# Performance work log

Measured on AMD Instinct MI355X. Metric: run time of the kernel, lower is better.

Reference implementation:

```python
import jax, jax.numpy as jnp
import numpy as np

GROUPS = 64; SIDE = 8; STEPS = 8
TAU = 1.0; FLOOR = 1e-4; EPS = 1e-4
MU = 1.0; DT = 0.1; GAMMA = 0.1
FLOW_W = 1.0; LOCAL_W = 0.5; KEEP_RATIO = 0.5


def _with_floor(m):
    n = m.shape[-1]
    mask = 1.0 - jnp.eye(n, dtype=m.dtype)
    return jnp.maximum(m * mask, FLOOR * mask)


def _norm_scores(s):
    mean = s.mean(axis=1, keepdims=True)
    std = jnp.clip(s.std(axis=1, ddof=1, keepdims=True), 1e-6, None)  # torch unbiased std
    return (s - mean) / std


def _router_core(tokens, cls_token, W, grid_h, grid_w):
    B, P, D = tokens.shape
    # group ids from patch grid position (patch_indices defaults to arange)
    pi = jnp.broadcast_to(jnp.arange(P), (B, P))
    row, col = pi // grid_w, pi % grid_w
    gh = -(-grid_h // SIDE); gw = -(-grid_w // SIDE)  # ceil div
    gid = jnp.minimum(row // gh, SIDE - 1) * SIDE + jnp.minimum(col // gw, SIDE - 1)  # [B,P]
    # mean-pool tokens per group (scatter_add + count)
    seg = jax.vmap(lambda t, g: jax.ops.segment_sum(t, g, num_segments=GROUPS))
    grouped = seg(tokens, gid)                                 # [B,G,D]
    counts = seg(jnp.ones((B, P, 1), tokens.dtype), gid)       # [B,G,1]
    grouped = grouped / jnp.maximum(counts, 1.0)
    nodes = jnp.concatenate([cls_token[:, None, :], grouped], axis=1)  # [B,G+1,D]
    # pairwise conductance: project, l2-normalize, squared cdist, exp kernel
    proj = jnp.einsum('bnd,ed->bne', nodes, W)  # Linear (no bias): x @ W.T
    proj = proj / jnp.maximum(jnp.linalg.norm(proj, axis=-1, keepdims=True), 1e-12)
    sq = jnp.sum(proj * proj, axis=-1)
    d2 = jnp.maximum(sq[:, :, None] + sq[:, None, :]
                     - 2.0 * jnp.einsum('bnd,bmd->bnm', proj, proj), 0.0)
    C = _with_floor(jnp.exp(-d2 / TAU))
    C = 0.5 * (C + jnp.swapaxes(C, -1, -2))  # symmetric
    # source: cls node injects, groups drain
    source = jnp.full((B, GROUPS + 1), -1.0 / GROUPS, C.dtype).at[:, 0].set(1.0)
    N = GROUPS + 1
    I = jnp.eye(N, dtype=C.dtype)
    d_list, q_list = [C], []
    for _ in range(STEPS):
        deg = C.sum(-1)
        system = deg[:, :, None] * I - C + EPS * I            # Laplacian + eps*I
        p = jnp.linalg.solve(system, source[..., None])[..., 0]
        flow = C * (p[:, :, None] - p[:, None, :])
        q_list.append(flow)
        r = jnp.abs(flow) ** MU
        r = r / (1.0 + r)
        C = C + DT * (r - GAMMA * C)
        C = _with_floor(jnp.maximum(C, 0.0))
        C = _with_floor(0.5 * (C + jnp.swapaxes(C, -1, -2)))
        d_list.append(C)
    return C, jnp.stack(d_list, 1), jnp.stack(q_list, 1), gid


def setup_inputs() -> dict:
    key = jax.random.key(0)
    k1, k2, k3, k4 = jax.random.split(key, 4)
    B, P, D = 64, 576, 768
    return {
        'tokens': jax.random.normal(k1, (B, P, D), jnp.float32),
        'cls_token': jax.random.normal(k2, (B, D), jnp.float32),
        'W': jax.random.normal(k3, (D, D), jnp.float32) / np.sqrt(D),
        'local_scores': jax.random.normal(k4, (B, P), jnp.float32),
        'grid_h': 24,
        'grid_w': 24,
    }


def reference(tokens, cls_token, W, local_scores, grid_h, grid_w):
    B, P, _ = tokens.shape
    final_d, d_hist, q_hist, gid = _router_core(tokens, cls_token, W, grid_h, grid_w)
    routing = final_d[:, 1:, 1:]
    routing = routing / jnp.clip(routing.sum(-1, keepdims=True), 1e-6, None)
    group_flow = jnp.abs(q_hist[:, -1, 1:, :]).sum(-1)        # [B,G]
    group_scores = jnp.take_along_axis(_norm_scores(group_flow), gid, axis=1)
    token_scores = FLOW_W * group_scores + LOCAL_W * _norm_scores(local_scores)
    keep_count = max(1, int(round(P * KEEP_RATIO)))
    _, topk = jax.lax.top_k(token_scores, keep_count)
    patch_keep_mask = jnp.zeros((B, P), bool).at[jnp.arange(B)[:, None], topk].set(True)
    keep_mask = jnp.concatenate([jnp.ones((B, 1), bool), patch_keep_mask], axis=1)
    delta = d_hist[:, 1:] - d_hist[:, :-1]
    aux_sparse = final_d[:, 1:, 1:].sum(axis=(-1, -2)).mean()
    aux_stable = jnp.abs(delta).sum(axis=(-1, -2, -3)).mean()
    return (keep_mask, patch_keep_mask, gid, group_scores, d_hist, q_hist,
            routing, aux_sparse, aux_stable)
```

## Files before the change

kernel.cpp:

```cpp
#include <hip/hip_runtime.h>
#include <stdint.h>

#define NB 64
#define NP 576
#define ND 768
#define NG 64
#define NN 65
#define NSTEPS 8
#define FLOORV 1.0e-4f
#define EPSV   1.0e-4f
#define DTV    0.1f
#define GAMMAV 0.1f
#define KEEPC  288
#define PITCH2 68

__global__ __launch_bounds__(256) void k_group_means(const float* __restrict__ tokens,
                                                     const float* __restrict__ cls,
                                                     float* __restrict__ nodes,
                                                     const int* __restrict__ ghp,
                                                     const int* __restrict__ gwp) {
    int bx = blockIdx.x;
    int b = bx / NN, n = bx - b * NN;
    int tid = threadIdx.x;
    float* orow = nodes + (size_t)bx * ND;
    if (n == 0) {
        for (int d = tid; d < ND; d += 256) orow[d] = cls[(size_t)b * ND + d];
        return;
    }
    int grid_h = *ghp, grid_w = *gwp;
    int gh = (grid_h + 7) / 8, gw = (grid_w + 7) / 8;
    int g = n - 1, gr = g >> 3, gc = g & 7;
    int r0 = gr * gh, r1 = (gr == 7) ? grid_h : min((gr + 1) * gh, grid_h);
    int c0 = gc * gw, c1 = (gc == 7) ? grid_w : min((gc + 1) * gw, grid_w);
    int cnt = (r1 > r0 && c1 > c0) ? (r1 - r0) * (c1 - c0) : 0;
    float cf = (float)max(cnt, 1);
    const float* tb = tokens + (size_t)b * NP * ND;
    for (int d = tid; d < ND; d += 256) {
        float acc = 0.f;
        for (int r = r0; r < r1; ++r)
            for (int c = c0; c < c1; ++c)
                acc += tb[(size_t)(r * grid_w + c) * ND + d];
        orow[d] = acc / cf;
    }
}

__global__ __launch_bounds__(256) void k_gemm_nt(const float* __restrict__ A,
                                                 const float* __restrict__ Bm,
                                                 float* __restrict__ Cm) {
    __shared__ float As[32][68];
    __shared__ float Bs[32][68];
    int tid = threadIdx.x;
    int m0 = blockIdx.x * 64, n0 = blockIdx.y * 64;
    int tx = tid & 15, ty = tid >> 4;
    float acc[4][4];
#pragma unroll
    for (int i = 0; i < 4; ++i)
#pragma unroll
        for (int j = 0; j < 4; ++j) acc[i][j] = 0.f;
    int lrow = tid >> 3, lq = tid & 7;
    for (int k0 = 0; k0 < ND; k0 += 32) {
#pragma unroll
        for (int l = 0; l < 2; ++l) {
            int row = lrow + l * 32;
            float4 va = *(const float4*)&A[(size_t)(m0 + row) * ND + k0 + lq * 4];
            As[lq * 4 + 0][row] = va.x; As[lq * 4 + 1][row] = va.y;
            As[lq * 4 + 2][row] = va.z; As[lq * 4 + 3][row] = va.w;
            float4 vb = *(const float4*)&Bm[(size_t)(n0 + row) * ND + k0 + lq * 4];
            Bs[lq * 4 + 0][row] = vb.x; Bs[lq * 4 + 1][row] = vb.y;
            Bs[lq * 4 + 2][row] = vb.z; Bs[lq * 4 + 3][row] = vb.w;
        }
        __syncthreads();
#pragma unroll
        for (int kk = 0; kk < 32; ++kk) {
            float4 a4 = *(const float4*)&As[kk][ty * 4];
            float4 b4 = *(const float4*)&Bs[kk][tx * 4];
            float av[4] = {a4.x, a4.y, a4.z, a4.w};
            float bv[4] = {b4.x, b4.y, b4.z, b4.w};
#pragma unroll
            for (int i = 0; i < 4; ++i)
#pragma unroll
                for (int j = 0; j < 4; ++j) acc[i][j] += av[i] * bv[j];
        }
        __syncthreads();
    }
#pragma unroll
    for (int i = 0; i < 4; ++i) {
        float4 o = make_float4(acc[i][0], acc[i][1], acc[i][2], acc[i][3]);
        *(float4*)&Cm[(size_t)(m0 + ty * 4 + i) * ND + n0 + tx * 4] = o;
    }
}

__global__ __launch_bounds__(256) void k_normalize(float* __restrict__ proj, float* __restrict__ sqv) {
    int r = blockIdx.x, tid = threadIdx.x;
    __shared__ double red[8];
    __shared__ float invs;
    float* row = proj + (size_t)r * ND;
    double s = 0.0;
    for (int d = tid; d < ND; d += 256) { double v = (double)row[d]; s += v * v; }
#pragma unroll
    for (int off = 32; off; off >>= 1) s += __shfl_down(s, off, 64);
    int wid = tid >> 6, lane = tid & 63;
    if (lane == 0) red[wid] = s;
    __syncthreads();
    if (tid == 0) invs = (float)(1.0 / fmax(sqrt(red[0] + red[1] + red[2] + red[3]), 1e-12));
    __syncthreads();
    float inv = invs;
    double s2 = 0.0;
    for (int d = tid; d < ND; d += 256) {
        float v = row[d] * inv; row[d] = v; s2 += (double)v * (double)v;
    }
#pragma unroll
    for (int off = 32; off; off >>= 1) s2 += __shfl_down(s2, off, 64);
    __syncthreads();
    if (lane == 0) red[wid] = s2;
    __syncthreads();
    if (tid == 0) sqv[r] = (float)(red[0] + red[1] + red[2] + red[3]);
}

__global__ __launch_bounds__(256) void k_pairwise(const float* __restrict__ proj,
                                                  const float* __restrict__ sqv,
                                                  float* __restrict__ dhist) {
    int b = blockIdx.x, tid = threadIdx.x;
    int tx = tid & 15, ty = tid >> 4;
    __shared__ float Ps[NN][65];
    float acc[5][5];
#pragma unroll
    for (int a = 0; a < 5; ++a)
#pragma unroll
        for (int c = 0; c < 5; ++c) acc[a][c] = 0.f;
    const float* Pb = proj + (size_t)b * NN * ND;
    for (int k0 = 0; k0 < ND; k0 += 64) {
        __syncthreads();
        for (int idx = tid; idx < NN * 64; idx += 256) {
            int i = idx >> 6, kk = idx & 63;
            Ps[i][kk] = Pb[(size_t)i * ND + k0 + kk];
        }
        __syncthreads();
        for (int kk = 0; kk < 64; ++kk) {
            float av[5], bv[5];
#pragma unroll
            for (int a = 0; a < 5; ++a) { int i = ty + 16 * a; av[a] = (i < NN) ? Ps[i][kk] : 0.f; }
#pragma unroll
            for (int c = 0; c < 5; ++c) { int j = tx + 16 * c; bv[c] = (j < NN) ? Ps[j][kk] : 0.f; }
#pragma unroll
            for (int a = 0; a < 5; ++a)
#pragma unroll
                for (int c = 0; c < 5; ++c) acc[a][c] += av[a] * bv[c];
        }
    }
#pragma unroll
    for (int a = 0; a < 5; ++a)
#pragma unroll
        for (int c = 0; c < 5; ++c) {
            int i = ty + 16 * a, j = tx + 16 * c;
            if (i < NN && j < NN) {
                float d2 = fmaxf(sqv[b * NN + i] + sqv[b * NN + j] - 2.0f * acc[a][c], 0.f);
                double cv = exp(-(double)d2);
                float cf = (i == j) ? 0.f : fmaxf((float)cv, FLOORV);
                dhist[(size_t)b * 9 * NN * NN + (size_t)i * NN + j] = cf;
            }
        }
}

__global__ __launch_bounds__(256) void k_dynamics(float* __restrict__ dhist,
                                                  float* __restrict__ qhist,
                                                  double* __restrict__ part) {
    int b = blockIdx.x, tid = threadIdx.x;
    __shared__ float Cs[NN * NN];
    __shared__ float Aug[NN * PITCH2];
    __shared__ float pd[NN];
    __shared__ double redd[8];
    float* C0 = dhist + (size_t)b * 9 * NN * NN;
    for (int t = tid; t < NN * NN; t += 256) Cs[t] = C0[t];
    __syncthreads();

    int r = tid >> 2, q = tid & 3;
    const int my_i = r + 1;
    float* mrow = Aug + my_i * PITCH2;
    double stable = 0.0, sparse = 0.0;

#pragma unroll 1
    for (int step = 0; step < NSTEPS; ++step) {
        for (int t = tid; t < NN * PITCH2; t += 256) {
            int i = t / PITCH2, j = t - i * PITCH2;
            if (j != i && j != NN)
                Aug[t] = (j < NN) ? -Cs[i * NN + j] : 0.f;
        }
        if (tid < NN) {
            float s = 0.f;
            const float* cr = Cs + tid * NN;
#pragma unroll 4
            for (int j = 0; j < NN; ++j) s += cr[j];
            Aug[tid * PITCH2 + tid] = s + EPSV;
            Aug[tid * PITCH2 + NN] = (tid == 0) ? 1.0f : (-1.0f / NG);
        }
        __syncthreads();

#pragma unroll 1
        for (int k = 0; k < NN - 1; k += 4) {
            float N4[4][4], Iv[4][4];
#pragma unroll
            for (int a = 0; a < 4; ++a)
#pragma unroll
                for (int c = 0; c < 4; ++c) {
                    N4[c][a] = Aug[(k + a) * PITCH2 + k + c];
                    Iv[c][a] = (a == c) ? 1.0f : 0.0f;
                }
#pragma unroll
            for (int p = 0; p < 4; ++p) {
                float ip = 1.0f / N4[p][p];
#pragma unroll
                for (int c = 0; c < 4; ++c) { N4[p][c] *= ip; Iv[p][c] *= ip; }
#pragma unroll
                for (int rr = 0; rr < 4; ++rr) {
                    if (rr != p) {
                        float f = N4[rr][p];
#pragma unroll
                        for (int c = 0; c < 4; ++c) {
                            N4[rr][c] -= f * N4[p][c];
                            Iv[rr][c] -= f * Iv[p][c];
                        }
                    }
                }
            }
            if (my_i >= k + 4) {
                float4 av = *(const float4*)(mrow + k);
                float x0 = Iv[0][0]*av.x + Iv[0][1]*av.y + Iv[0][2]*av.z + Iv[0][3]*av.w;
                float x1 = Iv[1][0]*av.x + Iv[1][1]*av.y + Iv[1][2]*av.z + Iv[1][3]*av.w;
                float x2 = Iv[2][0]*av.x + Iv[2][1]*av.y + Iv[2][2]*av.z + Iv[2][3]*av.w;
                float x3 = Iv[3][0]*av.x + Iv[3][1]*av.y + Iv[3][2]*av.z + Iv[3][3]*av.w;
                const float4* P0 = (const float4*)(Aug + (k + 0) * PITCH2);
                const float4* P1 = (const float4*)(Aug + (k + 1) * PITCH2);
                const float4* P2 = (const float4*)(Aug + (k + 2) * PITCH2);
                const float4* P3 = (const float4*)(Aug + (k + 3) * PITCH2);
                float4* M4 = (float4*)mrow;
#pragma unroll
                for (int u = 0; u < 5; ++u) {
                    int t = q + 4 * u;
                    if (t < 17) {
                        float4 m = M4[t];
                        float4 p0 = P0[t], p1 = P1[t], p2 = P2[t], p3 = P3[t];
                        m.x -= x0 * p0.x + x1 * p1.x + x2 * p2.x + x3 * p3.x;
                        m.y -= x0 * p0.y + x1 * p1.y + x2 * p2.y + x3 * p3.y;
                        m.z -= x0 * p0.z + x1 * p1.z + x2 * p2.z + x3 * p3.z;
                        m.w -= x0 * p0.w + x1 * p1.w + x2 * p2.w + x3 * p3.w;
                        M4[t] = m;
                    }
                }
            }
            __syncthreads();
        }

        {
            int g = tid >> 4, l16 = tid & 15;
            int base = g << 2;
            float* R0 = Aug + base * PITCH2;
            float* R1 = R0 + PITCH2;
            float* R2 = R1 + PITCH2;
            float* R3 = R2 + PITCH2;
            float4* R1v = (float4*)R1; float4* R2v = (float4*)R2; float4* R3v = (float4*)R3;
            const float4* R0v = (const float4*)R0;
            float inv0 = 1.0f / R0[base];
            float l10 = R1[base] * inv0;
            { float4 a = R1v[l16], p = R0v[l16];
              a.x -= l10*p.x; a.y -= l10*p.y; a.z -= l10*p.z; a.w -= l10*p.w; R1v[l16] = a; }
            if (l16 == 0) { float4 a = R1v[16], p = R0v[16];
              a.x -= l10*p.x; a.y -= l10*p.y; a.z -= l10*p.z; a.w -= l10*p.w; R1v[16] = a; }
            __syncthreads();
            float l20 = R2[base] * inv0;
            float l21 = (R2[base+1] - l20 * R0[base+1]) / R1[base+1];
            { float4 a = R2v[l16], p = R0v[l16], t1 = R1v[l16];
              a.x -= l20*p.x + l21*t1.x; a.y -= l20*p.y + l21*t1.y;
              a.z -= l20*p.z + l21*t1.z; a.w -= l20*p.w + l21*t1.w; R2v[l16] = a; }
            if (l16 == 0) { float4 a = R2v[16], p = R0v[16], t1 = R1v[16];
              a.x -= l20*p.x + l21*t1.x; a.y -= l20*p.y + l21*t1.y;
              a.z -= l20*p.z + l21*t1.z; a.w -= l20*p.w + l21*t1.w; R2v[16] = a; }
            __syncthreads();
            float l30 = R3[base] * inv0;
            float l31 = (R3[base+1] - l30 * R0[base+1]) / R1[base+1];
            float l32 = (R3[base+2] - l30 * R0[base+2] - l31 * R1[base+2]) / R2[base+2];
            { float4 a = R3v[l16], p = R0v[l16], t1 = R1v[l16], t2 = R2v[l16];
              a.x -= l30*p.x + l31*t1.x + l32*t2.x; a.y -= l30*p.y + l31*t1.y + l32*t2.y;
              a.z -= l30*p.z + l31*t1.z + l32*t2.z; a.w -= l30*p.w + l31*t1.w + l32*t2.w; R3v[l16] = a; }
            if (l16 == 0) { float4 a = R3v[16], p = R0v[16], t1 = R1v[16], t2 = R2v[16];
              a.x -= l30*p.x + l31*t1.x + l32*t2.x; a.y -= l30*p.y + l31*t1.y + l32*t2.y;
              a.z -= l30*p.z + l31*t1.z + l32*t2.z; a.w -= l30*p.w + l31*t1.w + l32*t2.w; R3v[16] = a; }
        }
        __syncthreads();

        if (tid < 64) {
            int lane = tid;
            int i_own = lane + 1;
            const float* brow = Aug + i_own * PITCH2;
            float inv_own = 1.0f / brow[i_own];
            float rhs = brow[NN];
            float acc = 0.f, p_own = 0.f;
#pragma unroll 2
            for (int i = NN - 1; i >= 1; --i) {
                float t = (rhs - acc) * inv_own;
                float pi = __shfl(t, i - 1, 64);
                if (i_own == i) p_own = t;
                acc += ((lane < i - 1) ? brow[i] : 0.f) * pi;
                if (lane == 0) pd[i] = pi;
            }
            float sp0 = Cs[i_own] * p_own;
#pragma unroll
            for (int off = 32; off; off >>= 1) sp0 += __shfl_down(sp0, off, 64);
            if (lane == 0) pd[0] = (1.0f + sp0) / Aug[0];
        }
        __syncthreads();

        float* qout = qhist + ((size_t)b * NSTEPS + step) * NN * NN;
        float* dout = dhist + ((size_t)b * 9 + step + 1) * NN * NN;
        for (int t = tid; t < NN * NN; t += 256) {
            int i = t / NN, j = t - i * NN;
            float c = Cs[t];
            float fl = c * (pd[i] - pd[j]);
            qout[t] = fl;
            float rr = fabsf(fl); rr = rr / (1.0f + rr);
            float cn = c + DTV * (rr - GAMMAV * c);
            float cnf = (i == j) ? 0.0f : fmaxf(cn, FLOORV);
            Cs[t] = cnf;
            dout[t] = cnf;
            stable += fabs((double)cnf - (double)c);
            if (step == NSTEPS - 1 && i > 0 && j > 0) sparse += (double)cnf;
        }
        __syncthreads();
    }

#pragma unroll
    for (int off = 32; off; off >>= 1) {
        stable += __shfl_down(stable, off, 64);
        sparse += __shfl_down(sparse, off, 64);
    }
    int wid = tid >> 6, lane = tid & 63;
    if (lane == 0) { redd[wid] = stable; redd[4 + wid] = sparse; }
    __syncthreads();
    if (tid == 0) {
        part[b]      = redd[4] + redd[5] + redd[6] + redd[7];
        part[NB + b] = redd[0] + redd[1] + redd[2] + redd[3];
    }
}

__global__ __launch_bounds__(256) void k_scores(const float* __restrict__ qhist,
                                                const float* __restrict__ local,
                                                const int* __restrict__ ghp,
                                                const int* __restrict__ gwp,
                                                float* __restrict__ keep,
                                                float* __restrict__ patch,
                                                float* __restrict__ gidout,
                                                float* __restrict__ gsout) {
    int b = blockIdx.x, tid = threadIdx.x;
    __shared__ double gf[NG];
    __shared__ double ts[NP];
    __shared__ double red[8];
    __shared__ double stats[2];
    if (tid < NG) {
        const float* qrow = qhist + ((size_t)b * NSTEPS + (NSTEPS - 1)) * NN * NN + (size_t)(tid + 1) * NN;
        double s = 0.0;
        for (int j = 0; j < NN; ++j) s += fabs((double)qrow[j]);
        gf[tid] = s;
    }
    __syncthreads();
    if (tid < 64) {
        double v = gf[tid];
        double s = v;
#pragma unroll
        for (int off = 32; off; off >>= 1) s += __shfl_down(s, off, 64);
        double mean = __shfl(s, 0, 64) / (double)NG;
        double d = v - mean, ss = d * d;
#pragma unroll
        for (int off = 32; off; off >>= 1) ss += __shfl_down(ss, off, 64);
        if (tid == 0) { stats[0] = mean; stats[1] = 1.0 / fmax(sqrt(ss / (NG - 1)), 1e-6); }
    }
    const float* lrow = local + (size_t)b * NP;
    double s1 = 0.0;
    for (int p = tid; p < NP; p += 256) s1 += (double)lrow[p];
#pragma unroll
    for (int off = 32; off; off >>= 1) s1 += __shfl_down(s1, off, 64);
    int wid = tid >> 6, lane = tid & 63;
    if (lane == 0) red[wid] = s1;
    __syncthreads();
    double lmean = (red[0] + red[1] + red[2] + red[3]) / (double)NP;
    double s2 = 0.0;
    for (int p = tid; p < NP; p += 256) { double d = (double)lrow[p] - lmean; s2 += d * d; }
#pragma unroll
    for (int off = 32; off; off >>= 1) s2 += __shfl_down(s2, off, 64);
    __syncthreads();
    if (lane == 0) red[wid] = s2;
    __syncthreads();
    double linv = 1.0 / fmax(sqrt((red[0] + red[1] + red[2] + red[3]) / (double)(NP - 1)), 1e-6);
    double gmean = stats[0], ginv = stats[1];
    int grid_h = *ghp, grid_w = *gwp;
    int gh = (grid_h + 7) / 8, gw = (grid_w + 7) / 8;
    for (int p = tid; p < NP; p += 256) {
        int row = p / grid_w, col = p - row * grid_w;
        int g = min(row / gh, 7) * 8 + min(col / gw, 7);
        double gsc = (gf[g] - gmean) * ginv;
        double lsc = ((double)lrow[p] - lmean) * linv;
        ts[p] = gsc + 0.5 * lsc;
        gidout[(size_t)b * NP + p] = (float)g;
        gsout[(size_t)b * NP + p]  = (float)gsc;
    }
    __syncthreads();
    for (int p = tid; p < NP; p += 256) {
        double sp = ts[p];
        int c = 0;
        for (int qq = 0; qq < NP; ++qq) {
            double v = ts[qq];
            c += (v > sp) || (v == sp && qq < p);
        }
        float kf = (c < KEEPC) ? 1.0f : 0.0f;
        patch[(size_t)b * NP + p] = kf;
        keep[(size_t)b * (NP + 1) + 1 + p] = kf;
    }
    if (tid == 0) keep[(size_t)b * (NP + 1)] = 1.0f;
}

__global__ void k_routing(const float* __restrict__ dhist, float* __restrict__ rout) {
    int b = blockIdx.x, tid = threadIdx.x;
    const float* Crow = dhist + ((size_t)b * 9 + 8) * NN * NN + (size_t)(tid + 1) * NN + 1;
    double s = 0.0;
    for (int j = 0; j < NG; ++j) s += (double)Crow[j];
    double inv = 1.0 / fmax(s, 1e-6);
    float* orow = rout + ((size_t)b * NG + tid) * NG;
    for (int j = 0; j < NG; ++j) orow[j] = (float)((double)Crow[j] * inv);
}

__global__ void k_aux(const double* __restrict__ part, float* __restrict__ osp, float* __restrict__ ost) {
    int tid = threadIdx.x;
    double sp = part[tid], st = part[NB + tid];
#pragma unroll
    for (int off = 32; off; off >>= 1) {
        sp += __shfl_down(sp, off, 64);
        st += __shfl_down(st, off, 64);
    }
    if (tid == 0) { *osp = (float)(sp / NB); *ost = (float)(st / NB); }
}

extern "C" void kernel_launch(void* const* d_in, const int* in_sizes, int n_in,
                              void* d_out, int out_size, void* d_ws, size_t ws_size,
                              hipStream_t stream) {
    const float* tokens = (const float*)d_in[0];
    const float* cls    = (const float*)d_in[1];
    const float* W      = (const float*)d_in[2];
    const float* local  = (const float*)d_in[3];
    const int* ghp = (const int*)d_in[4];
    const int* gwp = (const int*)d_in[5];

    float* out = (float*)d_out;
    float* o_keep  = out;
    float* o_patch = o_keep + (size_t)NB * (NP + 1);
    float* o_gid   = o_patch + (size_t)NB * NP;
    float* o_gs    = o_gid + (size_t)NB * NP;
    float* o_dh    = o_gs + (size_t)NB * NP;
    float* o_qh    = o_dh + (size_t)NB * 9 * NN * NN;
    float* o_rt    = o_qh + (size_t)NB * NSTEPS * NN * NN;
    float* o_sp    = o_rt + (size_t)NB * NG * NG;
    float* o_st    = o_sp + 1;

    float* nodes = (float*)d_ws;
    float* proj  = nodes + (size_t)NB * NN * ND;
    float* sqv   = proj + (size_t)NB * NN * ND;
    double* part = (double*)(((uintptr_t)(sqv + NB * NN) + 15) & ~(uintptr_t)15);

    k_group_means<<<NB * NN, 256, 0, stream>>>(tokens, cls, nodes, ghp, gwp);
    dim3 g2((NB * NN) / 64, ND / 64);
    k_gemm_nt<<<g2, 256, 0, stream>>>(nodes, W, proj);
    k_normalize<<<NB * NN, 256, 0, stream>>>(proj, sqv);
    k_pairwise<<<NB, 256, 0, stream>>>(proj, sqv, o_dh);
    k_dynamics<<<NB, 256, 0, stream>>>(o_dh, o_qh, part);
    k_scores<<<NB, 256, 0, stream>>>(o_qh, local, ghp, gwp, o_keep, o_patch, o_gid, o_gs);
    k_routing<<<NB, 64, 0, stream>>>(o_dh, o_rt);
    k_aux<<<1, 64, 0, stream>>>(part, o_sp, o_st);
}
```

Baseline: 683.2 us.

## Solve Laplacian system in registers within one wavefront using readlane

Replaces the shared-memory blocked Gauss-Jordan elimination, which needed a block-wide barrier after every 4-column panel, with a single-wavefront register-resident elimination. Each of 64 lanes holds one row (indices 1..64) in a register array, eliminates node 0 analytically first, then does forward elimination by broadcasting pivot rows with readlane, followed by back substitution. This removes the Aug shared buffer and most __syncthreads. In exchange, only one wave of the 256-thread block works during the solve, the per-lane 66-float array raises register pressure, and the fully unrolled 64x65 loops produce a very large instruction stream.

```diff
diff --git a/kernel.cpp b/kernel.cpp
--- a/kernel.cpp
+++ b/kernel.cpp
@@ -12,7 +12,6 @@
 #define DTV    0.1f
 #define GAMMAV 0.1f
 #define KEEPC  288
-#define PITCH2 68
 
 __global__ __launch_bounds__(256) void k_group_means(const float* __restrict__ tokens,
                                                      const float* __restrict__ cls,
@@ -162,151 +161,83 @@
         }
 }
 
+__device__ __forceinline__ float rl(float v, int l) {
+    return __int_as_float(__builtin_amdgcn_readlane(__float_as_int(v), l));
+}
+
 __global__ __launch_bounds__(256) void k_dynamics(float* __restrict__ dhist,
                                                   float* __restrict__ qhist,
                                                   double* __restrict__ part) {
     int b = blockIdx.x, tid = threadIdx.x;
     __shared__ float Cs[NN * NN];
-    __shared__ float Aug[NN * PITCH2];
     __shared__ float pd[NN];
     __shared__ double redd[8];
     float* C0 = dhist + (size_t)b * 9 * NN * NN;
     for (int t = tid; t < NN * NN; t += 256) Cs[t] = C0[t];
     __syncthreads();
 
-    int r = tid >> 2, q = tid & 3;
-    const int my_i = r + 1;
-    float* mrow = Aug + my_i * PITCH2;
+    const int lane = tid;
+    const int i_own = tid + 1;
     double stable = 0.0, sparse = 0.0;
 
 #pragma unroll 1
     for (int step = 0; step < NSTEPS; ++step) {
-        for (int t = tid; t < NN * PITCH2; t += 256) {
-            int i = t / PITCH2, j = t - i * PITCH2;
-            if (j != i && j != NN)
-                Aug[t] = (j < NN) ? -Cs[i * NN + j] : 0.f;
-        }
-        if (tid < NN) {
-            float s = 0.f;
-            const float* cr = Cs + tid * NN;
-#pragma unroll 4
-            for (int j = 0; j < NN; ++j) s += cr[j];
-            Aug[tid * PITCH2 + tid] = s + EPSV;
-            Aug[tid * PITCH2 + NN] = (tid == 0) ? 1.0f : (-1.0f / NG);
-        }
-        __syncthreads();
-
-#pragma unroll 1
-        for (int k = 0; k < NN - 1; k += 4) {
-            float N4[4][4], Iv[4][4];
-#pragma unroll
-            for (int a = 0; a < 4; ++a)
-#pragma unroll
-                for (int c = 0; c < 4; ++c) {
-                    N4[c][a] = Aug[(k + a) * PITCH2 + k + c];
-                    Iv[c][a] = (a == c) ? 1.0f : 0.0f;
-                }
-#pragma unroll
-            for (int p = 0; p < 4; ++p) {
-                float ip = 1.0f / N4[p][p];
-#pragma unroll
-                for (int c = 0; c < 4; ++c) { N4[p][c] *= ip; Iv[p][c] *= ip; }
-#pragma unroll
-                for (int rr = 0; rr < 4; ++rr) {
-                    if (rr != p) {
-                        float f = N4[rr][p];
-#pragma unroll
-                        for (int c = 0; c < 4; ++c) {
-                            N4[rr][c] -= f * N4[p][c];
-                            Iv[rr][c] -= f * Iv[p][c];
-                        }
-                    }
+        if (tid < 64) {
+            const float* crow = Cs + (size_t)i_own * NN;
+            float A_[66];
+            float deg = 0.f, c0 = 0.f;
+#pragma unroll
+            for (int j = 0; j < 65; ++j) {
+                float cv = crow[j];
+                deg += cv;
+                if (j == 0) c0 = cv; else A_[j] = -cv;
+            }
+            float diag = deg + EPSV;
+#pragma unroll
+            for (int j = 1; j < 65; ++j) A_[j] = (j == i_own) ? diag : A_[j];
+            A_[65] = -(1.0f / 64.0f);
+
+            float v0 = Cs[lane + 1];
+            float s0 = v0;
+#pragma unroll
+            for (int off = 1; off < 64; off <<= 1) s0 += __shfl_xor(s0, off, 64);
+            float d0 = s0 + EPSV;
+            float invd0 = 1.0f / d0;
+            float l0 = -c0 * invd0;
+#pragma unroll
+            for (int j = 1; j < 65; ++j)
+                A_[j] = __builtin_fmaf(l0, rl(v0, j - 1), A_[j]);
+            A_[65] -= l0;
+
+            float inv_own = 0.f;
+#pragma unroll
+            for (int k = 1; k < 65; ++k) {
+                float pk = rl(A_[k], k - 1);
+                float invp = 1.0f / pk;
+                inv_own = (lane == k - 1) ? invp : inv_own;
+                if (k < 64) {
+                    float l = (lane >= k) ? A_[k] * invp : 0.f;
+                    float ln = -l;
+#pragma unroll
+                    for (int j = k + 1; j < 66; ++j)
+                        A_[j] = __builtin_fmaf(ln, rl(A_[j], k - 1), A_[j]);
                 }
             }
-            if (my_i >= k + 4) {
-                float4 av = *(const float4*)(mrow + k);
-                float x0 = Iv[0][0]*av.x + Iv[0][1]*av.y + Iv[0][2]*av.z + Iv[0][3]*av.w;
-                float x1 = Iv[1][0]*av.x + Iv[1][1]*av.y + Iv[1][2]*av.z + Iv[1][3]*av.w;
-                float x2 = Iv[2][0]*av.x + Iv[2][1]*av.y + Iv[2][2]*av.z + Iv[2][3]*av.w;
-                float x3 = Iv[3][0]*av.x + Iv[3][1]*av.y + Iv[3][2]*av.z + Iv[3][3]*av.w;
-                const float4* P0 = (const float4*)(Aug + (k + 0) * PITCH2);
-                const float4* P1 = (const float4*)(Aug + (k + 1) * PITCH2);
-                const float4* P2 = (const float4*)(Aug + (k + 2) * PITCH2);
-                const float4* P3 = (const float4*)(Aug + (k + 3) * PITCH2);
-                float4* M4 = (float4*)mrow;
-#pragma unroll
-                for (int u = 0; u < 5; ++u) {
-                    int t = q + 4 * u;
-                    if (t < 17) {
-                        float4 m = M4[t];
-                        float4 p0 = P0[t], p1 = P1[t], p2 = P2[t], p3 = P3[t];
-                        m.x -= x0 * p0.x + x1 * p1.x + x2 * p2.x + x3 * p3.x;
-                        m.y -= x0 * p0.y + x1 * p1.y + x2 * p2.y + x3 * p3.y;
-                        m.z -= x0 * p0.z + x1 * p1.z + x2 * p2.z + x3 * p3.z;
-                        m.w -= x0 * p0.w + x1 * p1.w + x2 * p2.w + x3 * p3.w;
-                        M4[t] = m;
-                    }
-                }
+
+            float rhs = A_[65];
+            float acc = 0.f, p_own = 0.f;
+#pragma unroll
+            for (int i = 64; i >= 1; --i) {
+                float t = (rhs - acc) * inv_own;
+                float pi = rl(t, i - 1);
+                p_own = (i_own == i) ? t : p_own;
+                acc = __builtin_fmaf((i_own < i) ? A_[i] : 0.f, pi, acc);
             }
-            __syncthreads();
-        }
-
-        {
-            int g = tid >> 4, l16 = tid & 15;
-            int base = g << 2;
-            float* R0 = Aug + base * PITCH2;
-            float* R1 = R0 + PITCH2;
-            float* R2 = R1 + PITCH2;
-            float* R3 = R2 + PITCH2;
-            float4* R1v = (float4*)R1; float4* R2v = (float4*)R2; float4* R3v = (float4*)R3;
-            const float4* R0v = (const float4*)R0;
-            float inv0 = 1.0f / R0[base];
-            float l10 = R1[base] * inv0;
-            { float4 a = R1v[l16], p = R0v[l16];
-              a.x -= l10*p.x; a.y -= l10*p.y; a.z -= l10*p.z; a.w -= l10*p.w; R1v[l16] = a; }
-            if (l16 == 0) { float4 a = R1v[16], p = R0v[16];
-              a.x -= l10*p.x; a.y -= l10*p.y; a.z -= l10*p.z; a.w -= l10*p.w; R1v[16] = a; }
-            __syncthreads();
-            float l20 = R2[base] * inv0;
-            float l21 = (R2[base+1] - l20 * R0[base+1]) / R1[base+1];
-            { float4 a = R2v[l16], p = R0v[l16], t1 = R1v[l16];
-              a.x -= l20*p.x + l21*t1.x; a.y -= l20*p.y + l21*t1.y;
-              a.z -= l20*p.z + l21*t1.z; a.w -= l20*p.w + l21*t1.w; R2v[l16] = a; }
-            if (l16 == 0) { float4 a = R2v[16], p = R0v[16], t1 = R1v[16];
-              a.x -= l20*p.x + l21*t1.x; a.y -= l20*p.y + l21*t1.y;
-              a.z -= l20*p.z + l21*t1.z; a.w -= l20*p.w + l21*t1.w; R2v[16] = a; }
-            __syncthreads();
-            float l30 = R3[base] * inv0;
-            float l31 = (R3[base+1] - l30 * R0[base+1]) / R1[base+1];
-            float l32 = (R3[base+2] - l30 * R0[base+2] - l31 * R1[base+2]) / R2[base+2];
-            { float4 a = R3v[l16], p = R0v[l16], t1 = R1v[l16], t2 = R2v[l16];
-              a.x -= l30*p.x + l31*t1.x + l32*t2.x; a.y -= l30*p.y + l31*t1.y + l32*t2.y;
-              a.z -= l30*p.z + l31*t1.z + l32*t2.z; a.w -= l30*p.w + l31*t1.w + l32*t2.w; R3v[l16] = a; }
-            if (l16 == 0) { float4 a = R3v[16], p = R0v[16], t1 = R1v[16], t2 = R2v[16];
-              a.x -= l30*p.x + l31*t1.x + l32*t2.x; a.y -= l30*p.y + l31*t1.y + l32*t2.y;
-              a.z -= l30*p.z + l31*t1.z + l32*t2.z; a.w -= l30*p.w + l31*t1.w + l32*t2.w; R3v[16] = a; }
-        }
-        __syncthreads();
-
-        if (tid < 64) {
-            int lane = tid;
-            int i_own = lane + 1;
-            const float* brow = Aug + i_own * PITCH2;
-            float inv_own = 1.0f / brow[i_own];
-            float rhs = brow[NN];
-            float acc = 0.f, p_own = 0.f;
-#pragma unroll 2
-            for (int i = NN - 1; i >= 1; --i) {
-                float t = (rhs - acc) * inv_own;
-                float pi = __shfl(t, i - 1, 64);
-                if (i_own == i) p_own = t;
-                acc += ((lane < i - 1) ? brow[i] : 0.f) * pi;
-                if (lane == 0) pd[i] = pi;
-            }
-            float sp0 = Cs[i_own] * p_own;
-#pragma unroll
-            for (int off = 32; off; off >>= 1) sp0 += __shfl_down(sp0, off, 64);
-            if (lane == 0) pd[0] = (1.0f + sp0) / Aug[0];
+            pd[i_own] = p_own;
+            float sp = v0 * p_own;
+#pragma unroll
+            for (int off = 1; off < 64; off <<= 1) sp += __shfl_xor(sp, off, 64);
+            if (lane == 0) pd[0] = (1.0f + sp) * invd0;
         }
         __syncthreads();
 
@@ -333,8 +264,8 @@
         stable += __shfl_down(stable, off, 64);
         sparse += __shfl_down(sparse, off, 64);
     }
-    int wid = tid >> 6, lane = tid & 63;
-    if (lane == 0) { redd[wid] = stable; redd[4 + wid] = sparse; }
+    int wid = tid >> 6, lane63 = tid & 63;
+    if (lane63 == 0) { redd[wid] = stable; redd[4 + wid] = sparse; }
     __syncthreads();
     if (tid == 0) {
         part[b]      = redd[4] + redd[5] + redd[6] + redd[7];
```

Measured after the change: 1.133 ms. 65.9% more time.
